# Kernel optimization log

Hardware: AMD Instinct MI355X
Metric: run time of the kernel (lower is better)

The kernel has to match this reference:

```python
import jax, jax.numpy as jnp
import numpy as np

B, D, T, H, C = 65536, 1024, 16, 128, 10


def setup_inputs() -> dict:
    key = jax.random.key(0)
    k1, k2, k3, k4, k5, k6 = jax.random.split(key, 6)
    x = jax.random.normal(k1, (B, D), dtype=jnp.float32)
    task_id = jax.random.randint(k2, (B,), 0, T, dtype=jnp.int32)
    # per-task head params (torch nn.Linear init scale ~ 1/sqrt(fan_in))
    W1 = jax.random.normal(k3, (T, D, H), dtype=jnp.float32) / np.sqrt(D)
    b1 = jax.random.normal(k4, (T, H), dtype=jnp.float32) * 0.01
    W2 = jax.random.normal(k5, (T, H, C), dtype=jnp.float32) / np.sqrt(H)
    b2 = jax.random.normal(k6, (T, C), dtype=jnp.float32) * 0.01
    return {"x": x, "task_id": task_id, "W1": W1, "b1": b1, "W2": W2, "b2": b2}


def reference(x, task_id, W1, b1, W2, b2):
    # Dense dispatch: run every head on every sample as one big GEMM
    # (x @ [T*H] concatenated weights), then select each sample's task head.
    # Same math as the torch per-task mask/gather/scatter loop (eval mode,
    # dropout is identity).
    h = jax.nn.relu(jnp.einsum('bd,tdh->bth', x, W1) + b1)      # [B,T,H]
    logits_all = jnp.einsum('bth,thc->btc', h, W2) + b2          # [B,T,C]
    # gather the row for each sample's task_id
    logits = jnp.take_along_axis(
        logits_all, task_id[:, None, None].astype(jnp.int32), axis=1
    ).squeeze(1)                                                 # [B,C]
    return logits
```

## Files before the change

kernel.cpp:

```cpp
#include <hip/hip_runtime.h>
#include <hip/hip_bf16.h>

#define TASKS 16
#define DIM 1024
#define HID 128
#define NCLS 10
#define NB 65536
#define BM 128
#define NTILES (NB / BM + TASKS)

typedef __attribute__((ext_vector_type(8))) short bf16x8;
typedef __attribute__((ext_vector_type(4))) float f32x4;
typedef __attribute__((ext_vector_type(2))) float f32x2;

__device__ __forceinline__ unsigned short f2bf(float f) {
    union { __hip_bfloat16 h; unsigned short s; } u; u.h = __float2bfloat16(f); return u.s;
}

__device__ __forceinline__ void glds16(const void* gsrc, void* ldst) {
    __builtin_amdgcn_global_load_lds(
        (const __attribute__((address_space(1))) unsigned*)gsrc,
        (__attribute__((address_space(3))) unsigned*)ldst, 16, 0, 0);
}


__global__ __launch_bounds__(256) void k_pre(const int* __restrict__ tid_arr,
                                             const float* __restrict__ W1,
                                             const float* __restrict__ W2,
                                             int* __restrict__ ws) {
    const int blk = blockIdx.x, tid = threadIdx.x;
    if (blk < 256) {
        __shared__ int l[TASKS];
        if (tid < TASKS) l[tid] = 0;
        __syncthreads();
        atomicAdd(&l[tid_arr[blk * 256 + tid]], 1);
        __syncthreads();
        if (tid < TASKS) atomicAdd(&ws[tid], l[tid]);
    } else if (blk < 768) {
        const int idx = blk - 256;
        const int t = idx >> 5, kt = idx & 31;
        char* dst = (char*)((short*)(ws + 64 + NB) + ((size_t)(t * 32 + kt) << 12));
        const float* wsrc = W1 + (size_t)t * DIM * HID;
        #pragma unroll
        for (int cch = 0; cch < 2; ++cch) {
            const int p = tid * 32 + cch * 16;
            const int col = p >> 6;
            const int lgk = ((p >> 4) & 3) ^ (col & 3);
            const int kbase = kt * 32 + lgk * 8;
            bf16x8 v;
            #pragma unroll
            for (int j = 0; j < 8; ++j)
                v[j] = (short)f2bf(wsrc[(size_t)(kbase + j) * HID + col]);
            *(bf16x8*)(dst + p) = v;
        }
    } else {
        const int t = blk - 768;
        short* W2t = (short*)(ws + 64 + NB) + ((size_t)TASKS * 32 * 4096);
        #pragma unroll
        for (int i = 0; i < 8; ++i) {
            const int o = i * 256 + tid, c = o >> 7, h = o & 127;
            const float v = (c < NCLS) ? W2[((size_t)t * HID + h) * NCLS + c] : 0.f;
            W2t[((size_t)t * 16 + c) * HID + h] = (short)f2bf(v);
        }
    }
}

__global__ __launch_bounds__(256) void k_scatter(const int* __restrict__ tid_arr,
                                                 int* __restrict__ ws) {
    __shared__ int l[TASKS], base[TASKS], off[TASKS];
    const int tid = threadIdx.x;
    if (tid < TASKS) l[tid] = 0;
    __syncthreads();
    const int i = blockIdx.x * 256 + tid;
    const int t = tid_arr[i];
    const int rank = atomicAdd(&l[t], 1);
    __syncthreads();
    if (tid == 0) {
        int ro = 0;
        for (int k = 0; k < TASKS; ++k) { off[k] = ro; ro += ws[k]; }
    }
    if (tid < TASKS && l[tid] > 0) base[tid] = atomicAdd(&ws[16 + tid], l[tid]);
    __syncthreads();
    ws[64 + off[t] + base[t] + rank] = i;
}

__global__ __launch_bounds__(256, 3) void k_main(
    const float* __restrict__ x, const float* __restrict__ b1,
    const float* __restrict__ b2, const int* __restrict__ ws,
    float* __restrict__ out)
{
    __shared__ __align__(16) short smem[16384];
    __shared__ int ridx[BM];

    const int* cnt = ws;
    const int* rowIdx = ws + 64;
    const short* W1s = (const short*)(ws + 64 + NB);
    const short* W2t = W1s + ((size_t)TASKS * 32 * 4096);

    const int w = (blockIdx.x & 7) * (NTILES / 8) + (blockIdx.x >> 3);

    int t = -1, m = 0, gstart = 0;
    {
        int accT = 0, accO = 0;
        for (int k = 0; k < TASKS; ++k) {
            const int c = cnt[k], nt = (c + BM - 1) >> 7;
            if (t < 0 && w < accT + nt) {
                t = k; gstart = accO + (w - accT) * BM;
                m = c - (w - accT) * BM; if (m > BM) m = BM;
            }
            accT += nt; accO += c;
        }
    }
    if (t < 0) return;

    const int tid = threadIdx.x;
    if (tid < BM) ridx[tid] = rowIdx[gstart + (tid < m ? tid : m - 1)];
    __syncthreads();

    const int lane = tid & 63, wv = tid >> 6;
    const int lg = lane >> 4, lr = lane & 15;
    const int wrow = (wv >> 1) * 64, wcol = (wv & 1) * 64;

    const float* gpA[8];
    unsigned wbA[8];
    #pragma unroll
    for (int j = 0; j < 8; ++j) {
        const int row = wv * 32 + j * 4 + lg;
        gpA[j] = x + ((size_t)ridx[row] << 10) + lr * 2;
        wbA[j] = row * 64 + (((lr >> 2) ^ lg) << 4) + (lr & 3) * 4;
    }
    const char* w1sT = (const char*)W1s + ((size_t)t << 18);
    const int bi = wv * 2;

    f32x2 a8[8];
    f32x4 acc[4][4] = {};
    const unsigned sw = (unsigned)((lg ^ (lr & 3)) << 4);

    auto LOADA = [&](int kt) {
        #pragma unroll
        for (int j = 0; j < 8; ++j) a8[j] = *(const f32x2*)(gpA[j] + kt * 32);
    };
    auto WRITEA = [&](int buf) {
        char* ab = (char*)smem + buf * 16384;
        #pragma unroll
        for (int j = 0; j < 8; ++j) {
            unsigned pk = ((unsigned)f2bf(a8[j][1]) << 16) | (unsigned)f2bf(a8[j][0]);
            *(unsigned*)(ab + wbA[j]) = pk;
        }
    };
    auto ISSUEB = [&](int buf, int kt) {
        const char* src = w1sT + ((size_t)kt << 13) + bi * 1024 + lane * 16;
        char* dst = (char*)smem + buf * 16384 + 8192 + bi * 1024;
        glds16(src, dst);
        glds16(src + 1024, dst + 1024);
    };
    auto COMPUTE = [&](int buf) {
        const char* ab = (const char*)smem + buf * 16384;
        const char* bb = ab + 8192;
        bf16x8 af[4], bfr[4];
        #pragma unroll
        for (int rf = 0; rf < 4; ++rf)
            af[rf] = *(const bf16x8*)(ab + (wrow + rf * 16 + lr) * 64 + sw);
        #pragma unroll
        for (int cf = 0; cf < 4; ++cf)
            bfr[cf] = *(const bf16x8*)(bb + (wcol + cf * 16 + lr) * 64 + sw);
        #pragma unroll
        for (int rf = 0; rf < 4; ++rf)
            #pragma unroll
            for (int cf = 0; cf < 4; ++cf)
                acc[rf][cf] = __builtin_amdgcn_mfma_f32_16x16x32_bf16(af[rf], bfr[cf], acc[rf][cf], 0, 0, 0);
    };

    ISSUEB(0, 0);
    LOADA(0);
    WRITEA(0);
    __syncthreads();
    #pragma unroll 2
    for (int kt = 0; kt < 32; ++kt) {
        const int buf = kt & 1;
        if (kt < 31) { ISSUEB(buf ^ 1, kt + 1); LOADA(kt + 1); }
        COMPUTE(buf);
        if (kt < 31) WRITEA(buf ^ 1);
        __syncthreads();
    }

    short* hl = smem;
    #pragma unroll
    for (int cf = 0; cf < 4; ++cf) {
        const int col = wcol + cf * 16 + lr;
        const float b1v = b1[t * HID + col];
        #pragma unroll
        for (int rf = 0; rf < 4; ++rf)
            #pragma unroll
            for (int q = 0; q < 4; ++q) {
                const int row = wrow + rf * 16 + lg * 4 + q;
                const float hv = fmaxf(acc[rf][cf][q] + b1v, 0.f);
                *(unsigned short*)((char*)hl + row * 256 +
                    (((col >> 3) ^ (row & 7)) << 4) + (col & 7) * 2) = f2bf(hv);
            }
    }
    __syncthreads();

    f32x4 acc2[2] = {};
    #pragma unroll
    for (int ks = 0; ks < 4; ++ks) {
        bf16x8 bvv = *(const bf16x8*)(W2t + (((size_t)t * 16 + lr) << 7) + ks * 32 + lg * 8);
        #pragma unroll
        for (int rf = 0; rf < 2; ++rf) {
            const int row = wv * 32 + rf * 16 + lr;
            bf16x8 avv = *(const bf16x8*)((const char*)hl + row * 256 +
                             (((ks * 4 + lg) ^ (row & 7)) << 4));
            acc2[rf] = __builtin_amdgcn_mfma_f32_16x16x32_bf16(avv, bvv, acc2[rf], 0, 0, 0);
        }
    }
    if (lr < NCLS) {
        const float b2v = b2[t * NCLS + lr];
        #pragma unroll
        for (int rf = 0; rf < 2; ++rf)
            #pragma unroll
            for (int q = 0; q < 4; ++q) {
                const int row = wv * 32 + rf * 16 + lg * 4 + q;
                if (row < m) out[(size_t)ridx[row] * NCLS + lr] = acc2[rf][q] + b2v;
            }
    }
}

extern "C" void kernel_launch(void* const* d_in, const int* in_sizes, int n_in,
                              void* d_out, int out_size, void* d_ws, size_t ws_size,
                              hipStream_t stream) {
    (void)in_sizes; (void)n_in; (void)out_size; (void)ws_size;
    const float* x       = (const float*)d_in[0];
    const int*   task_id = (const int*)d_in[1];
    const float* W1      = (const float*)d_in[2];
    const float* b1      = (const float*)d_in[3];
    const float* W2      = (const float*)d_in[4];
    const float* b2      = (const float*)d_in[5];
    float* out = (float*)d_out;
    int* ws = (int*)d_ws;
    hipMemsetAsync(ws, 0, 128, stream);
    k_pre<<<784, 256, 0, stream>>>(task_id, W1, W2, ws);
    k_scatter<<<256, 256, 0, stream>>>(task_id, ws);
    k_main<<<NTILES, 256, 0, stream>>>(x, b1, b2, ws, out);
}
```

Measured before the change: 90.03 us.

## Stage W1 transpose through LDS, widen x loads, raise occupancy, replace memset

The W1 bf16 conversion now reads a 32x128 slab of W1 coalesced into padded shared memory and then transposes it from LDS, replacing the strided global reads. In the main kernel each thread loads 16-byte float4 chunks of x instead of 8-byte pairs (4 loads instead of 8) and writes 8-byte packed bf16 to LDS with an adjusted swizzle. The launch bound minimum blocks per CU goes from 3 to 4, which may force register spilling. The hipMemsetAsync is replaced by a tiny zeroing kernel to cut launch overhead.

```diff
diff --git a/kernel.cpp b/kernel.cpp
--- a/kernel.cpp
+++ b/kernel.cpp
@@ -11,7 +11,7 @@
 
 typedef __attribute__((ext_vector_type(8))) short bf16x8;
 typedef __attribute__((ext_vector_type(4))) float f32x4;
-typedef __attribute__((ext_vector_type(2))) float f32x2;
+typedef __attribute__((ext_vector_type(2))) unsigned u32x2;
 
 __device__ __forceinline__ unsigned short f2bf(float f) {
     union { __hip_bfloat16 h; unsigned short s; } u; u.h = __float2bfloat16(f); return u.s;
@@ -23,6 +23,10 @@
         (__attribute__((address_space(3))) unsigned*)ldst, 16, 0, 0);
 }
 
+
+__global__ void k_zero(int* __restrict__ ws) {
+    if (threadIdx.x < 32) ws[threadIdx.x] = 0;
+}
 
 __global__ __launch_bounds__(256) void k_pre(const int* __restrict__ tid_arr,
                                              const float* __restrict__ W1,
@@ -39,19 +43,24 @@
     } else if (blk < 768) {
         const int idx = blk - 256;
         const int t = idx >> 5, kt = idx & 31;
+        __shared__ float ld[32 * 132];
+        const float* src = W1 + ((size_t)t * DIM + kt * 32) * HID;
+        #pragma unroll
+        for (int r = 0; r < 16; ++r) {
+            const int fl = r * 256 + tid;
+            ld[(fl >> 7) * 132 + (fl & 127)] = src[fl];
+        }
+        __syncthreads();
         char* dst = (char*)((short*)(ws + 64 + NB) + ((size_t)(t * 32 + kt) << 12));
-        const float* wsrc = W1 + (size_t)t * DIM * HID;
-        #pragma unroll
-        for (int cch = 0; cch < 2; ++cch) {
-            const int p = tid * 32 + cch * 16;
-            const int col = p >> 6;
-            const int lgk = ((p >> 4) & 3) ^ (col & 3);
-            const int kbase = kt * 32 + lgk * 8;
+        const int col = tid >> 1, half = tid & 1;
+        #pragma unroll
+        for (int g = 0; g < 2; ++g) {
+            const int lgk = (half * 2 + g) ^ (col & 3);
             bf16x8 v;
             #pragma unroll
             for (int j = 0; j < 8; ++j)
-                v[j] = (short)f2bf(wsrc[(size_t)(kbase + j) * HID + col]);
-            *(bf16x8*)(dst + p) = v;
+                v[j] = (short)f2bf(ld[(lgk * 8 + j) * 132 + col]);
+            *(bf16x8*)(dst + tid * 32 + g * 16) = v;
         }
     } else {
         const int t = blk - 768;
@@ -84,7 +93,7 @@
     ws[64 + off[t] + base[t] + rank] = i;
 }
 
-__global__ __launch_bounds__(256, 3) void k_main(
+__global__ __launch_bounds__(256, 4) void k_main(
     const float* __restrict__ x, const float* __restrict__ b1,
     const float* __restrict__ b2, const int* __restrict__ ws,
     float* __restrict__ out)
@@ -121,31 +130,33 @@
     const int lg = lane >> 4, lr = lane & 15;
     const int wrow = (wv >> 1) * 64, wcol = (wv & 1) * 64;
 
-    const float* gpA[8];
-    unsigned wbA[8];
+    const float* gpA[4];
+    unsigned wbA[4];
     #pragma unroll
-    for (int j = 0; j < 8; ++j) {
-        const int row = wv * 32 + j * 4 + lg;
-        gpA[j] = x + ((size_t)ridx[row] << 10) + lr * 2;
-        wbA[j] = row * 64 + (((lr >> 2) ^ lg) << 4) + (lr & 3) * 4;
+    for (int j = 0; j < 4; ++j) {
+        const int row = wv * 32 + j * 8 + (lane >> 3);
+        gpA[j] = x + ((size_t)ridx[row] << 10) + (lane & 7) * 4;
+        wbA[j] = row * 64 + ((((lane & 7) >> 1) ^ (row & 3)) << 4) + (lane & 1) * 8;
     }
     const char* w1sT = (const char*)W1s + ((size_t)t << 18);
     const int bi = wv * 2;
 
-    f32x2 a8[8];
+    f32x4 a8[4];
     f32x4 acc[4][4] = {};
     const unsigned sw = (unsigned)((lg ^ (lr & 3)) << 4);
 
     auto LOADA = [&](int kt) {
         #pragma unroll
-        for (int j = 0; j < 8; ++j) a8[j] = *(const f32x2*)(gpA[j] + kt * 32);
+        for (int j = 0; j < 4; ++j) a8[j] = *(const f32x4*)(gpA[j] + kt * 32);
     };
     auto WRITEA = [&](int buf) {
         char* ab = (char*)smem + buf * 16384;
         #pragma unroll
-        for (int j = 0; j < 8; ++j) {
-            unsigned pk = ((unsigned)f2bf(a8[j][1]) << 16) | (unsigned)f2bf(a8[j][0]);
-            *(unsigned*)(ab + wbA[j]) = pk;
+        for (int j = 0; j < 4; ++j) {
+            u32x2 pk;
+            pk[0] = ((unsigned)f2bf(a8[j][1]) << 16) | (unsigned)f2bf(a8[j][0]);
+            pk[1] = ((unsigned)f2bf(a8[j][3]) << 16) | (unsigned)f2bf(a8[j][2]);
+            *(u32x2*)(ab + wbA[j]) = pk;
         }
     };
     auto ISSUEB = [&](int buf, int kt) {
@@ -237,7 +248,7 @@
     const float* b2      = (const float*)d_in[5];
     float* out = (float*)d_out;
     int* ws = (int*)d_ws;
-    hipMemsetAsync(ws, 0, 128, stream);
+    k_zero<<<1, 64, 0, stream>>>(ws);
     k_pre<<<784, 256, 0, stream>>>(task_id, W1, W2, ws);
     k_scatter<<<256, 256, 0, stream>>>(task_id, ws);
     k_main<<<NTILES, 256, 0, stream>>>(x, b1, b2, ws, out);
```

Measured after the change: 85.67 us. 4.8% less time.
